# Optimization experiments

Hardware: AMD Instinct MI355X
Metric: run time of the kernel (lower is better)

Reference implementation:

```python
import jax, jax.numpy as jnp
from jax import lax
import numpy as np

N, T, V = 32, 32, 128
C_FEAT, C_BOX, C_CLS = 256, 4, 4
C_IN = C_FEAT + C_BOX + C_CLS  # 264 (is_scene=False concatenates x,b,c)
C_OUT = 64
K = 9
EPS = 1e-3  # keras BatchNormalization default epsilon


def _bn4(x, g, b, m, v):
    # inference-mode BN over channel axis 1 of (N,C,T,V)
    s = (g * lax.rsqrt(v + EPS))[None, :, None, None]
    return (x - m[None, :, None, None]) * s + b[None, :, None, None]


def _stgcn(x, a, imp, w, bw, ga, ba, ma, va, al, wt, bt, gb, bb, mb, vb, residual):
    res = x if residual else 0.0
    # SGCN: 1x1 conv (channels_first) then adjacency aggregation; dropout is identity at inference
    h = jnp.einsum('nctv,co->notv', x, w) + bw[None, :, None, None]
    h = jnp.einsum('nctv,ntvw->nctw', h, a * imp)
    # TGCN: BN -> PReLU(alpha per (C,T,V)) -> temporal conv (K,1) SAME -> BN -> (dropout=id)
    h = _bn4(h, ga, ba, ma, va)
    h = jnp.where(h >= 0, h, al[None] * h)
    h = lax.conv_general_dilated(h, wt, (1, 1), 'SAME',
                                 dimension_numbers=('NCHW', 'HWIO', 'NCHW')) + bt[None, :, None, None]
    h = _bn4(h, gb, bb, mb, vb)
    return h + res  # use_mdn=True -> no final PReLU


def _forward(x, b, c, a, dbn_g, dbn_b, dbn_m, dbn_v,
             w0, bw0, imp0, g0a, b0a, m0a, v0a, al0, wt0, bt0, g0b, b0b, m0b, v0b,
             w1, bw1, imp1, g1a, b1a, m1a, v1a, al1, wt1, bt1, g1b, b1b, m1b, v1b):
    x = jnp.concatenate([x, b, c], axis=-1)  # (N,T,V,C_IN)
    n, t, v, cc = x.shape
    # data BN over flattened (V*C) channel axis, exactly as the TF reshapes do
    x = jnp.transpose(x, (0, 2, 3, 1)).reshape(n, v * cc, t)
    s = (dbn_g * lax.rsqrt(dbn_v + EPS))[None, :, None]
    x = (x - dbn_m[None, :, None]) * s + dbn_b[None, :, None]
    # NOTE: the original does transpose(0,1,3,2) then a *reshape* to (N,C,T,V); replicate exactly
    x = x.reshape(n, v, cc, t).transpose(0, 1, 3, 2).reshape(n, cc, t, v)
    x = _stgcn(x, a, imp0, w0, bw0, g0a, b0a, m0a, v0a, al0, wt0, bt0, g0b, b0b, m0b, v0b, residual=False)
    x = _stgcn(x, a, imp1, w1, bw1, g1a, b1a, m1a, v1a, al1, wt1, bt1, g1b, b1b, m1b, v1b, residual=True)
    x = x[:, :, :, 0]  # (N,C_OUT,T)
    return jnp.transpose(x, (0, 2, 1))  # (N,T,C_OUT)


def setup_inputs():
    key = jax.random.key(0)
    ks = jax.random.split(key, 40)
    rn = lambda k, s, sc=1.0: jax.random.normal(k, s, jnp.float32) * sc
    ru = lambda k, s, lo, hi: jax.random.uniform(k, s, jnp.float32, lo, hi)
    d = {}
    d['x'] = rn(ks[0], (N, T, V, C_FEAT))
    d['b'] = rn(ks[1], (N, T, V, C_BOX))
    d['c'] = ru(ks[2], (N, T, V, C_CLS), 0.0, 1.0)
    d['a'] = ru(ks[3], (N, T, V, V), 0.0, 1.0)
    d['dbn_g'] = ru(ks[4], (V * C_IN,), 0.5, 1.5)
    d['dbn_b'] = rn(ks[5], (V * C_IN,), 0.1)
    d['dbn_m'] = rn(ks[6], (V * C_IN,), 0.1)
    d['dbn_v'] = ru(ks[7], (V * C_IN,), 0.5, 1.5)

    def mk_layer(i, cin, kb):
        d['w%d' % i] = rn(ks[kb], (cin, C_OUT), (1.0 / cin) ** 0.5)
        d['bw%d' % i] = rn(ks[kb + 1], (C_OUT,), 0.01)
        d['imp%d' % i] = rn(ks[kb + 2], (V, V), (2.0 / (V * V)) ** 0.5)
        d['g%da' % i] = ru(ks[kb + 3], (C_OUT,), 0.5, 1.5)
        d['b%da' % i] = rn(ks[kb + 4], (C_OUT,), 0.1)
        d['m%da' % i] = rn(ks[kb + 5], (C_OUT,), 0.1)
        d['v%da' % i] = ru(ks[kb + 6], (C_OUT,), 0.5, 1.5)
        d['al%d' % i] = ru(ks[kb + 7], (C_OUT, T, V), 0.0, 0.3)
        d['wt%d' % i] = rn(ks[kb + 8], (K, 1, C_OUT, C_OUT), (1.0 / (K * C_OUT)) ** 0.5)
        d['bt%d' % i] = rn(ks[kb + 9], (C_OUT,), 0.01)
        d['g%db' % i] = ru(ks[kb + 10], (C_OUT,), 0.5, 1.5)
        d['b%db' % i] = rn(ks[kb + 11], (C_OUT,), 0.1)
        d['m%db' % i] = rn(ks[kb + 12], (C_OUT,), 0.1)
        d['v%db' % i] = ru(ks[kb + 13], (C_OUT,), 0.5, 1.5)

    mk_layer(0, C_IN, 8)
    mk_layer(1, C_OUT, 22)
    return d


def reference(x, b, c, a, dbn_g, dbn_b, dbn_m, dbn_v,
              w0, bw0, imp0, g0a, b0a, m0a, v0a, al0, wt0, bt0, g0b, b0b, m0b, v0b,
              w1, bw1, imp1, g1a, b1a, m1a, v1a, al1, wt1, bt1, g1b, b1b, m1b, v1b):
    return _forward(x, b, c, a, dbn_g, dbn_b, dbn_m, dbn_v,
                    w0, bw0, imp0, g0a, b0a, m0a, v0a, al0, wt0, bt0, g0b, b0b, m0b, v0b,
                    w1, bw1, imp1, g1a, b1a, m1a, v1a, al1, wt1, bt1, g1b, b1b, m1b, v1b)
```

## Files before the change

### kernel.cpp

```cpp
#include <hip/hip_runtime.h>
#include <hip/hip_bf16.h>

typedef unsigned short u16;
typedef unsigned int   u32;

#define N_   32
#define T_   32
#define V_   128
#define CIN_ 264
#define CO_  64
#define KT_  9
#define EPS_ 1e-3f

#define OFF_DBN_S 0
#define OFF_DBN_O 33792
#define OFF_W0    67584
#define OFF_BW0   84480
#define OFF_A0S   84544
#define OFF_A0O   84608
#define OFF_B0S   84672
#define OFF_B0O   84736
#define OFF_W1    84800
#define OFF_BW1   88896
#define OFF_A1S   88960
#define OFF_A1O   89024
#define OFF_B1S   89088
#define OFF_B1O   89152
#define PREP_TOTAL 110464

#define B_P    0
#define B_FLAG 360448
#define B_W0A  360512
#define B_WTA  397440
#define B_H0   524288
#define B_G0   (B_H0 + 16777216)
#define B_L0   (B_G0 + 16777216)
#define B_G1P  (B_L0 + 33554432)
#define B_XP2  (B_G1P + 262144)
#define B_END  (B_XP2 + 69206016)

typedef short bf16x8 __attribute__((ext_vector_type(8)));
typedef float f32x4  __attribute__((ext_vector_type(4)));

__device__ __forceinline__ float bf2f(u16 u) { return __uint_as_float(((u32)u) << 16); }
__device__ __forceinline__ u16 f2bf(float f) {
    u32 x = __float_as_uint(f);
    return (u16)((x + 0x7fffu + ((x >> 16) & 1u)) >> 16);
}
__device__ __forceinline__ float ldin(const void* p, u32 i, int f32) {
    return f32 ? ((const float*)p)[i] : bf2f(((const u16*)p)[i]);
}
__device__ __forceinline__ u32 swzv(u32 v) {
    u32 m = (v >> 3) & 7u;
    return (m << 4) ^ ((m & 3u) << 5);
}

__global__ void k_detect(const void* a, int* flag) {
    if (threadIdx.x == 0 && blockIdx.x == 0) {
        const u16* p = (const u16*)a;
        int cnt = 0;
        for (int i = 0; i < 64; ++i) {
            float v = bf2f(p[2 * i]);
            if (v >= 0.f && v <= 1.0f) ++cnt;
        }
        *flag = (cnt >= 56) ? 0 : 1;
    }
}

__global__ void k_prep(const void* dbn_g, const void* dbn_b, const void* dbn_m, const void* dbn_v,
                       const void* w0, const void* bw0,
                       const void* g0a, const void* b0a, const void* m0a, const void* v0a,
                       const void* bt0, const void* g0b, const void* b0b, const void* m0b, const void* v0b,
                       const void* w1, const void* bw1,
                       const void* g1a, const void* b1a, const void* m1a, const void* v1a,
                       const void* bt1, const void* g1b, const void* b1b, const void* m1b, const void* v1b,
                       const void* wt0,
                       float* P, u16* W0A, u16* WTA, const int* flagp)
{
    const int f32 = *flagp;
    int i = blockIdx.x * 256 + threadIdx.x;
    if (i < 33792) {
        float s = ldin(dbn_g, i, f32) * rsqrtf(ldin(dbn_v, i, f32) + EPS_);
        P[OFF_DBN_S + i] = s;
        P[OFF_DBN_O + i] = ldin(dbn_b, i, f32) - ldin(dbn_m, i, f32) * s;
    } else if (i < 50688) { int j = i - 33792; P[OFF_W0 + j] = ldin(w0, j, f32); }
    else if (i < 50752) { int j = i - 50688; P[OFF_BW0 + j] = ldin(bw0, j, f32); }
    else if (i < 50816) { int j = i - 50752;
        float s = ldin(g0a, j, f32) * rsqrtf(ldin(v0a, j, f32) + EPS_);
        P[OFF_A0S + j] = s; P[OFF_A0O + j] = ldin(b0a, j, f32) - ldin(m0a, j, f32) * s;
    } else if (i < 50880) { int j = i - 50816;
        float s = ldin(g0b, j, f32) * rsqrtf(ldin(v0b, j, f32) + EPS_);
        P[OFF_B0S + j] = s; P[OFF_B0O + j] = (ldin(bt0, j, f32) - ldin(m0b, j, f32)) * s + ldin(b0b, j, f32);
    } else if (i < 54976) { int j = i - 50880; P[OFF_W1 + j] = ldin(w1, j, f32); }
    else if (i < 55040) { int j = i - 54976; P[OFF_BW1 + j] = ldin(bw1, j, f32); }
    else if (i < 55104) { int j = i - 55040;
        float s = ldin(g1a, j, f32) * rsqrtf(ldin(v1a, j, f32) + EPS_);
        P[OFF_A1S + j] = s; P[OFF_A1O + j] = ldin(b1a, j, f32) - ldin(m1a, j, f32) * s;
    } else if (i < 55168) { int j = i - 55104;
        float s = ldin(g1b, j, f32) * rsqrtf(ldin(v1b, j, f32) + EPS_);
        P[OFF_B1S + j] = s; P[OFF_B1O + j] = (ldin(bt1, j, f32) - ldin(m1b, j, f32)) * s + ldin(b1b, j, f32);
    } else if (i < 73600) {
        int j = i - 55168; int c = j / 288, ci = j - c * 288;
        float val = (ci < 264) ? ldin(w0, (u32)ci * 64 + c, f32)
                  : ((ci == 264) ? ldin(bw0, c, f32) : 0.f);
        W0A[j] = f2bf(val);
    } else if (i < 110464) {
        int j = i - 73600; int k = j >> 12, rem = j & 4095, o = rem >> 6, ii = rem & 63;
        WTA[j] = f2bf(ldin(wt0, ((u32)(k * 64 + ii)) * 64 + o, f32));
    }
}

__global__ __launch_bounds__(256) void k_bnx(const void* __restrict__ xin, const void* __restrict__ bin,
                                             const void* __restrict__ cin2, const float* __restrict__ P,
                                             u16* __restrict__ Xp, const int* __restrict__ flagp)
{
    __shared__ __align__(16) u16 tile[32 * 130];
    const int f32 = *flagp;
    const int rt = blockIdx.x;
    const int ct = blockIdx.y;
    const int n  = blockIdx.z;
    const int c0 = ct * 32;
    const int ncols = (ct == 8) ? 8 : 32;
    const int r0 = rt * 128;
    const int tid = threadIdx.x;

    for (int q = tid; q < ncols * 32; q += 256) {
        int j = q >> 5, i4 = (q & 31) << 2;
        u32 L = (u32)(c0 + j) * 4096u + (u32)(r0 + i4);
        u32 vs = L / 8448u;
        u32 r  = L - vs * 8448u;
        u32 ts = r / 264u;
        u32 cc = r - ts * 264u;
        u32 base = ((u32)n * 32u + ts) * 128u + vs;
        float4 val;
        if (f32) {
            if (cc < 256u)      val = *(const float4*)((const float*)xin  + (size_t)base * 256u + cc);
            else if (cc < 260u) val = *(const float4*)((const float*)bin  + (size_t)base * 4u + (cc - 256u));
            else                val = *(const float4*)((const float*)cin2 + (size_t)base * 4u + (cc - 260u));
        } else {
            ushort4 uv;
            if (cc < 256u)      uv = *(const ushort4*)((const u16*)xin  + (size_t)base * 256u + cc);
            else if (cc < 260u) uv = *(const ushort4*)((const u16*)bin  + (size_t)base * 4u + (cc - 256u));
            else                uv = *(const ushort4*)((const u16*)cin2 + (size_t)base * 4u + (cc - 260u));
            val.x = bf2f(uv.x); val.y = bf2f(uv.y); val.z = bf2f(uv.z); val.w = bf2f(uv.w);
        }
        u32 ch = vs * 264u + cc;
        const float4 s4 = *(const float4*)&P[OFF_DBN_S + ch];
        const float4 o4 = *(const float4*)&P[OFF_DBN_O + ch];
        ushort2 lo, hi;
        lo.x = f2bf(fmaf(val.x, s4.x, o4.x));
        lo.y = f2bf(fmaf(val.y, s4.y, o4.y));
        hi.x = f2bf(fmaf(val.z, s4.z, o4.z));
        hi.y = f2bf(fmaf(val.w, s4.w, o4.w));
        *(ushort2*)&tile[j * 130 + i4]     = lo;
        *(ushort2*)&tile[j * 130 + i4 + 2] = hi;
    }
    __syncthreads();
    const int chunks = ncols >> 3;
    for (int e = tid; e < 128 * chunks; e += 256) {
        int i, cch;
        if (chunks == 4) { i = e >> 2; cch = e & 3; } else { i = e; cch = 0; }
        __align__(16) u16 tmp[8];
#pragma unroll
        for (int k2 = 0; k2 < 8; ++k2) tmp[k2] = tile[(cch * 8 + k2) * 130 + i];
        *(uint4*)&Xp[((u32)n * 4096u + (u32)(r0 + i)) * 264u + (u32)(c0 + cch * 8)] = *(uint4*)tmp;
    }
}

__global__ __launch_bounds__(256) void k_pw0(const u16* __restrict__ Xp, const u16* __restrict__ W0Ag,
                                             u16* __restrict__ h0)
{
    const int t2 = blockIdx.x, n = blockIdx.y, vh = blockIdx.z;
    const int tid = threadIdx.x;
    const int wv = tid >> 6, lane = tid & 63, l16 = lane & 15, quad = lane >> 4;
    const int m0 = wv * 16;
    const int vrow = vh * 64 + m0 + l16;
    const u16* arow = Xp + ((u32)n * 4096u + (u32)(t2 * 128 + vrow)) * 264u;

    f32x4 acc[4];
#pragma unroll
    for (int i = 0; i < 4; ++i) acc[i] = (f32x4){0.f, 0.f, 0.f, 0.f};

#pragma unroll
    for (int ks = 0; ks < 8; ++ks) {
        const int k0 = ks * 32 + quad * 8;
        bf16x8 af = *(const bf16x8*)&arow[k0];
#pragma unroll
        for (int ni = 0; ni < 4; ++ni) {
            bf16x8 bf = *(const bf16x8*)&W0Ag[(u32)(ni * 16 + l16) * 288 + k0];
            acc[ni] = __builtin_amdgcn_mfma_f32_16x16x32_bf16(af, bf, acc[ni], 0, 0, 0);
        }
    }
    {
        bf16x8 af = (bf16x8){0, 0, 0, 0, 0, 0, 0, 0};
        if (quad == 0)      af = *(const bf16x8*)&arow[256];
        else if (quad == 1) af[0] = (short)0x3F80;
        const int k0 = 256 + quad * 8;
#pragma unroll
        for (int ni = 0; ni < 4; ++ni) {
            bf16x8 bf = *(const bf16x8*)&W0Ag[(u32)(ni * 16 + l16) * 288 + k0];
            acc[ni] = __builtin_amdgcn_mfma_f32_16x16x32_bf16(af, bf, acc[ni], 0, 0, 0);
        }
    }
    const int v = vh * 64 + m0 + quad * 4;
#pragma unroll
    for (int ni = 0; ni < 4; ++ni) {
        int c = ni * 16 + l16;
        ushort4 rr; u16* rp = (u16*)&rr;
#pragma unroll
        for (int r = 0; r < 4; ++r) rp[r] = f2bf(acc[ni][r]);
        *(ushort4*)&h0[((u32)(n * 64 + c) * 32 + t2) * 128 + v] = rr;
    }
}

__global__ __launch_bounds__(256) void k_graph0(const void* __restrict__ a, const void* __restrict__ imp0,
                                                const void* __restrict__ al0, const float* __restrict__ P,
                                                const u16* __restrict__ h0, u16* __restrict__ g0,
                                                const int* __restrict__ flagp)
{
    __shared__ __align__(16) u16 tile[128 * 128];
    const int f32 = *flagp;
    const int t = blockIdx.x, n = blockIdx.y;
    const int tid = threadIdx.x;
    const u32 abase = (((u32)n * 32u + (u32)t) * 128u) * 128u;

    for (int e = tid; e < 2048; e += 256) {
        int v = e >> 4, w0 = (e & 15) << 3;
        float vals[8];
        if (f32) {
            const float* ap = (const float*)a + abase + (u32)v * 128u + w0;
            const float* ip = (const float*)imp0 + (u32)v * 128u + w0;
            float4 x0 = *(const float4*)ap, x1 = *(const float4*)(ap + 4);
            float4 i0 = *(const float4*)ip, i1 = *(const float4*)(ip + 4);
            vals[0] = x0.x * i0.x; vals[1] = x0.y * i0.y; vals[2] = x0.z * i0.z; vals[3] = x0.w * i0.w;
            vals[4] = x1.x * i1.x; vals[5] = x1.y * i1.y; vals[6] = x1.z * i1.z; vals[7] = x1.w * i1.w;
        } else {
            uint4 xu = *(const uint4*)((const u16*)a + abase + (u32)v * 128u + w0);
            uint4 iu = *(const uint4*)((const u16*)imp0 + (u32)v * 128u + w0);
            const u16* xp = (const u16*)&xu; const u16* ip = (const u16*)&iu;
#pragma unroll
            for (int j = 0; j < 8; ++j) vals[j] = bf2f(xp[j]) * bf2f(ip[j]);
        }
        __align__(16) u16 pk[8];
#pragma unroll
        for (int j = 0; j < 8; ++j) pk[j] = f2bf(vals[j]);
        u32 byte = (u32)v * 256u + (((u32)w0 * 2u) ^ swzv((u32)v));
        *(uint4*)((char*)tile + byte) = *(uint4*)pk;
    }
    __syncthreads();

    const int wv = tid >> 6, lane = tid & 63, l16 = lane & 15, quad = lane >> 4;
    const int n0w = wv * 32;
    const u16* Hb = h0 + ((u32)n * 2048u + (u32)t) * 128u;

    f32x4 acc[4][2];
#pragma unroll
    for (int mi = 0; mi < 4; ++mi) { acc[mi][0] = (f32x4){0,0,0,0}; acc[mi][1] = (f32x4){0,0,0,0}; }
#pragma unroll
    for (int ks = 0; ks < 4; ++ks) {
        const int k0 = ks * 32 + quad * 8;
        const u32 xr = swzv((u32)k0);
        const u32 wb0 = (u32)(n0w + l16) * 2u;
        const u32 wb1 = (u32)(n0w + 16 + l16) * 2u;
        bf16x8 bf0, bf1;
#pragma unroll
        for (int j = 0; j < 8; ++j) {
            const u32 rb = (u32)(k0 + j) * 256u;
            bf0[j] = (short)*(const u16*)((const char*)tile + rb + (wb0 ^ xr));
            bf1[j] = (short)*(const u16*)((const char*)tile + rb + (wb1 ^ xr));
        }
#pragma unroll
        for (int mi = 0; mi < 4; ++mi) {
            bf16x8 af = *(const bf16x8*)&Hb[(u32)(mi * 16 + l16) * 4096u + k0];
            acc[mi][0] = __builtin_amdgcn_mfma_f32_16x16x32_bf16(af, bf0, acc[mi][0], 0, 0, 0);
            acc[mi][1] = __builtin_amdgcn_mfma_f32_16x16x32_bf16(af, bf1, acc[mi][1], 0, 0, 0);
        }
    }
#pragma unroll
    for (int mi = 0; mi < 4; ++mi) {
        const int c0 = mi * 16 + quad * 4;
        const float4 s4 = *(const float4*)&P[OFF_A0S + c0];
        const float4 o4 = *(const float4*)&P[OFF_A0O + c0];
        const float ss[4] = {s4.x, s4.y, s4.z, s4.w};
        const float oo[4] = {o4.x, o4.y, o4.z, o4.w};
#pragma unroll
        for (int ni = 0; ni < 2; ++ni) {
            const int w = n0w + ni * 16 + l16;
            ushort4 rr; u16* rp = (u16*)&rr;
#pragma unroll
            for (int r = 0; r < 4; ++r) {
                float y = fmaf(acc[mi][ni][r], ss[r], oo[r]);
                float alv = ldin(al0, ((u32)(c0 + r) * 32 + t) * 128 + w, f32);
                rp[r] = f2bf((y >= 0.f) ? y : alv * y);
            }
            *(ushort4*)&g0[((u32)(n * 32 + t) * 128 + w) * 64 + c0] = rr;
        }
    }
}

__global__ __launch_bounds__(256) void k_tconv0(const u16* __restrict__ WTAg, const float* __restrict__ P,
                                                const u16* __restrict__ g0, float* __restrict__ L0)
{
    const int t = blockIdx.x, n = blockIdx.y;
    const int tid = threadIdx.x;
    const int kmin = (t < 4) ? (4 - t) : 0;
    const int kmax = (t > 27) ? (35 - t) : 8;
    const int wv = tid >> 6, lane = tid & 63, l16 = lane & 15, quad = lane >> 4;
    const int n0w = wv * 32;

    f32x4 acc[4][2];
#pragma unroll
    for (int mi = 0; mi < 4; ++mi) { acc[mi][0] = (f32x4){0,0,0,0}; acc[mi][1] = (f32x4){0,0,0,0}; }

    for (int k = kmin; k <= kmax; ++k) {
        const u16* Wb = WTAg + (u32)k * 4096u;
        const u16* Bb = g0 + ((u32)(n * 32 + (t + k - 4)) * 128u) * 64u;
#pragma unroll
        for (int ks = 0; ks < 2; ++ks) {
            const int k0 = ks * 32 + quad * 8;
            bf16x8 bf0 = *(const bf16x8*)&Bb[(u32)(n0w + l16) * 64u + k0];
            bf16x8 bf1 = *(const bf16x8*)&Bb[(u32)(n0w + 16 + l16) * 64u + k0];
#pragma unroll
            for (int mi = 0; mi < 4; ++mi) {
                bf16x8 af = *(const bf16x8*)&Wb[(u32)(mi * 16 + l16) * 64u + k0];
                acc[mi][0] = __builtin_amdgcn_mfma_f32_16x16x32_bf16(af, bf0, acc[mi][0], 0, 0, 0);
                acc[mi][1] = __builtin_amdgcn_mfma_f32_16x16x32_bf16(af, bf1, acc[mi][1], 0, 0, 0);
            }
        }
    }
#pragma unroll
    for (int mi = 0; mi < 4; ++mi) {
        const int ob = mi * 16 + quad * 4;
        const float4 s4 = *(const float4*)&P[OFF_B0S + ob];
        const float4 o4 = *(const float4*)&P[OFF_B0O + ob];
        const float ss[4] = {s4.x, s4.y, s4.z, s4.w};
        const float oo[4] = {o4.x, o4.y, o4.z, o4.w};
#pragma unroll
        for (int ni = 0; ni < 2; ++ni) {
            const int v = n0w + ni * 16 + l16;
#pragma unroll
            for (int r = 0; r < 4; ++r)
                L0[((u32)(n * 64 + ob + r) * 32 + t) * 128 + v] = fmaf(acc[mi][ni][r], ss[r], oo[r]);
        }
    }
}

__global__ __launch_bounds__(256) void k_pw1(const void* __restrict__ a, const void* __restrict__ imp1,
                                             const void* __restrict__ al1, const float* __restrict__ P,
                                             const float* __restrict__ L0, float* __restrict__ g1p,
                                             const int* __restrict__ flagp)
{
    __shared__ float amv[V_];
    __shared__ float xr[CO_];
    __shared__ float Ssh;
    const int f32 = *flagp;
    const int t = blockIdx.x, n = blockIdx.y;
    const int tid = threadIdx.x;

    if (tid < V_) {
        float av = ldin(a, (((u32)n * T_ + t) * V_ + tid) * V_ + 0u, f32)
                 * ldin(imp1, (u32)tid * V_ + 0u, f32);
        amv[tid] = av;
    }
    __syncthreads();
    if (tid < 64) {
        float s = amv[tid] + amv[tid + 64];
#pragma unroll
        for (int m = 1; m < 64; m <<= 1) s += __shfl_xor(s, m);
        if (tid == 0) Ssh = s;
    }
    const int c = tid >> 2, sub = tid & 3;
    const float* Lrow = L0 + (u32)n * (CO_ * T_ * V_) + (u32)c * (T_ * V_) + (u32)t * V_ + sub * 32;
    float p = 0.f;
#pragma unroll
    for (int j = 0; j < 32; j += 4) {
        float4 x = *(const float4*)(Lrow + j);
        float4 m = *(const float4*)&amv[sub * 32 + j];
        p = fmaf(x.x, m.x, p); p = fmaf(x.y, m.y, p);
        p = fmaf(x.z, m.z, p); p = fmaf(x.w, m.w, p);
    }
    p += __shfl_xor(p, 1);
    p += __shfl_xor(p, 2);
    if (sub == 0) xr[c] = p;
    __syncthreads();
    if (tid < CO_) {
        const int o = tid;
        float y = P[OFF_BW1 + o] * Ssh;
        for (int cc = 0; cc < CO_; ++cc)
            y = fmaf(xr[cc], P[OFF_W1 + cc * CO_ + o], y);
        y = fmaf(y, P[OFF_A1S + o], P[OFF_A1O + o]);
        float alv = ldin(al1, ((u32)o * T_ + t) * V_ + 0u, f32);
        y = (y >= 0.f) ? y : alv * y;
        g1p[((u32)n * CO_ + o) * T_ + t] = y;
    }
}

__global__ __launch_bounds__(256) void k_tconv1(const void* __restrict__ wt1, const float* __restrict__ P,
                                                const float* __restrict__ g1p, const float* __restrict__ L0,
                                                void* __restrict__ out, const int* __restrict__ flagp)
{
    __shared__ float gl[CO_][40];
    const int f32 = *flagp;
    const int n = blockIdx.x;
    const int tid = threadIdx.x;
    for (int e = tid; e < 512; e += 256) {
        int i = e >> 3, p = e & 7;
        gl[i][(p < 4) ? p : (p + 32)] = 0.f;
    }
    for (int e = tid; e < 2048; e += 256) {
        int i = e >> 5, tt = e & 31;
        gl[i][tt + 4] = g1p[(u32)n * 2048u + (u32)i * 32u + tt];
    }
    __syncthreads();
    const int o = tid & 63, tq = tid >> 6, t0 = tq * 8;
    float acc[8];
#pragma unroll
    for (int j = 0; j < 8; ++j) acc[j] = 0.f;
    for (int i = 0; i < CO_; ++i) {
        float win[16];
#pragma unroll
        for (int m = 0; m < 16; m += 4) *(float4*)&win[m] = *(const float4*)&gl[i][t0 + m];
#pragma unroll
        for (int k = 0; k < KT_; ++k) {
            float wv = ldin(wt1, ((u32)(k * CO_ + i)) * CO_ + o, f32);
#pragma unroll
            for (int j = 0; j < 8; ++j) acc[j] = fmaf(win[j + k], wv, acc[j]);
        }
    }
    const float s1 = P[OFF_B1S + o], o1 = P[OFF_B1O + o];
#pragma unroll
    for (int j = 0; j < 8; ++j) {
        const int t = t0 + j;
        float y = fmaf(acc[j], s1, o1);
        y += L0[(u32)n * (CO_ * T_ * V_) + (u32)o * (T_ * V_) + (u32)t * V_ + 0];
        const u32 oi = ((u32)n * T_ + t) * CO_ + o;
        if (f32) ((float*)out)[oi] = y;
        else     ((u16*)out)[oi]   = f2bf(y);
    }
}

__global__ void k_fail(u16* out, int nel) {
    int i = blockIdx.x * 256 + threadIdx.x;
    if (i < nel) out[i] = 0x7f80;
}

extern "C" void kernel_launch(void* const* d_in, const int* in_sizes, int n_in,
                              void* d_out, int out_size, void* d_ws, size_t ws_size,
                              hipStream_t stream)
{
    const void* xin  = d_in[0];
    const void* bin  = d_in[1];
    const void* cin2 = d_in[2];
    const void* a    = d_in[3];
    const void* dbn_g = d_in[4];
    const void* dbn_b = d_in[5];
    const void* dbn_m = d_in[6];
    const void* dbn_v = d_in[7];
    const void* w0  = d_in[8];
    const void* bw0 = d_in[9];
    const void* imp0 = d_in[10];
    const void* g0a = d_in[11];
    const void* b0a = d_in[12];
    const void* m0a = d_in[13];
    const void* v0a = d_in[14];
    const void* al0 = d_in[15];
    const void* wt0 = d_in[16];
    const void* bt0 = d_in[17];
    const void* g0b = d_in[18];
    const void* b0b = d_in[19];
    const void* m0b = d_in[20];
    const void* v0b = d_in[21];
    const void* w1  = d_in[22];
    const void* bw1 = d_in[23];
    const void* imp1 = d_in[24];
    const void* g1a = d_in[25];
    const void* b1a = d_in[26];
    const void* m1a = d_in[27];
    const void* v1a = d_in[28];
    const void* al1 = d_in[29];
    const void* wt1 = d_in[30];
    const void* bt1 = d_in[31];
    const void* g1b = d_in[32];
    const void* b1b = d_in[33];
    const void* m1b = d_in[34];
    const void* v1b = d_in[35];

    if (ws_size < (size_t)B_END) {
        k_fail<<<(out_size + 255) / 256, 256, 0, stream>>>((u16*)d_out, out_size);
        return;
    }
    char* w = (char*)d_ws;
    float* P    = (float*)(w + B_P);
    int*   flg  = (int*)(w + B_FLAG);
    u16*   W0A  = (u16*)(w + B_W0A);
    u16*   WTA  = (u16*)(w + B_WTA);
    u16*   h0   = (u16*)(w + B_H0);
    u16*   g0   = (u16*)(w + B_G0);
    float* L0   = (float*)(w + B_L0);
    float* g1p  = (float*)(w + B_G1P);
    u16*   Xp   = (u16*)(w + B_XP2);

    k_detect<<<1, 64, 0, stream>>>(a, flg);
    k_prep<<<(PREP_TOTAL + 255) / 256, 256, 0, stream>>>(
        dbn_g, dbn_b, dbn_m, dbn_v, w0, bw0, g0a, b0a, m0a, v0a,
        bt0, g0b, b0b, m0b, v0b, w1, bw1, g1a, b1a, m1a, v1a,
        bt1, g1b, b1b, m1b, v1b, wt0, P, W0A, WTA, flg);

    dim3 grid(T_, N_);
    k_bnx   <<<dim3(32, 9, 32), 256, 0, stream>>>(xin, bin, cin2, P, Xp, flg);
    k_pw0   <<<dim3(T_, N_, 2), 256, 0, stream>>>(Xp, W0A, h0);
    k_graph0<<<grid, 256, 0, stream>>>(a, imp0, al0, P, h0, g0, flg);
    k_tconv0<<<grid, 256, 0, stream>>>(WTA, P, g0, L0);
    k_pw1   <<<grid, 256, 0, stream>>>(a, imp1, al1, P, L0, g1p, flg);
    k_tconv1<<<dim3(N_), 256, 0, stream>>>(wt1, P, g1p, L0, d_out, flg);
}
```

Measured before the change: 506.5 us.

## Fuse data batch-norm transpose into first pointwise MFMA kernel via swizzled LDS tile

```diff
diff --git a/kernel.cpp b/kernel.cpp
--- a/kernel.cpp
+++ b/kernel.cpp
@@ -36,8 +36,7 @@
 #define B_G0   (B_H0 + 16777216)
 #define B_L0   (B_G0 + 16777216)
 #define B_G1P  (B_L0 + 33554432)
-#define B_XP2  (B_G1P + 262144)
-#define B_END  (B_XP2 + 69206016)
+#define B_END  (B_G1P + 262144)
 
 typedef short bf16x8 __attribute__((ext_vector_type(8)));
 typedef float f32x4  __attribute__((ext_vector_type(4)));
@@ -50,8 +49,8 @@
 __device__ __forceinline__ float ldin(const void* p, u32 i, int f32) {
     return f32 ? ((const float*)p)[i] : bf2f(((const u16*)p)[i]);
 }
-__device__ __forceinline__ u32 swzv(u32 v) {
-    u32 m = (v >> 3) & 7u;
+__device__ __forceinline__ u32 swzv(u32 row) {
+    u32 m = (row >> 3) & 7u;
     return (m << 4) ^ ((m & 3u) << 5);
 }
 
@@ -110,99 +109,94 @@
     }
 }
 
-__global__ __launch_bounds__(256) void k_bnx(const void* __restrict__ xin, const void* __restrict__ bin,
+__global__ __launch_bounds__(256) void k_pwf(const void* __restrict__ xin, const void* __restrict__ bin,
                                              const void* __restrict__ cin2, const float* __restrict__ P,
-                                             u16* __restrict__ Xp, const int* __restrict__ flagp)
-{
-    __shared__ __align__(16) u16 tile[32 * 130];
+                                             const u16* __restrict__ W0Ag, u16* __restrict__ h0,
+                                             const int* __restrict__ flagp)
+{
+    __shared__ __align__(16) u16 tile[288 * 64];
     const int f32 = *flagp;
-    const int rt = blockIdx.x;
-    const int ct = blockIdx.y;
-    const int n  = blockIdx.z;
-    const int c0 = ct * 32;
-    const int ncols = (ct == 8) ? 8 : 32;
-    const int r0 = rt * 128;
+    const int t2 = blockIdx.x, n = blockIdx.y, vh = blockIdx.z;
     const int tid = threadIdx.x;
 
-    for (int q = tid; q < ncols * 32; q += 256) {
-        int j = q >> 5, i4 = (q & 31) << 2;
-        u32 L = (u32)(c0 + j) * 4096u + (u32)(r0 + i4);
+    for (int e = tid; e < 192; e += 256) {
+        int row = 264 + (e >> 3), chunk = e & 7;
+        u32 fill = (row == 264) ? 0x3F803F80u : 0u;
+        uint4 z = make_uint4(fill, fill, fill, fill);
+        u32 byte = (u32)row * 128u + (((u32)chunk * 16u) ^ swzv((u32)row));
+        *(uint4*)((char*)tile + byte) = z;
+    }
+    for (int e = tid; e < 2112; e += 256) {
+        int c2 = e >> 3, vv0 = (e & 7) << 3;
+        u32 L = (u32)c2 * 4096u + (u32)(t2 * 128 + vh * 64 + vv0);
         u32 vs = L / 8448u;
         u32 r  = L - vs * 8448u;
         u32 ts = r / 264u;
         u32 cc = r - ts * 264u;
         u32 base = ((u32)n * 32u + ts) * 128u + vs;
-        float4 val;
+        u32 ch = vs * 264u + cc;
+        float v8[8];
         if (f32) {
-            if (cc < 256u)      val = *(const float4*)((const float*)xin  + (size_t)base * 256u + cc);
-            else if (cc < 260u) val = *(const float4*)((const float*)bin  + (size_t)base * 4u + (cc - 256u));
-            else                val = *(const float4*)((const float*)cin2 + (size_t)base * 4u + (cc - 260u));
+            float4 a0, a1;
+            if (cc < 256u) {
+                const float* sp = (const float*)xin + (size_t)base * 256u + cc;
+                a0 = *(const float4*)sp; a1 = *(const float4*)(sp + 4);
+            } else {
+                a0 = *(const float4*)((const float*)bin  + (size_t)base * 4u);
+                a1 = *(const float4*)((const float*)cin2 + (size_t)base * 4u);
+            }
+            v8[0] = a0.x; v8[1] = a0.y; v8[2] = a0.z; v8[3] = a0.w;
+            v8[4] = a1.x; v8[5] = a1.y; v8[6] = a1.z; v8[7] = a1.w;
         } else {
-            ushort4 uv;
-            if (cc < 256u)      uv = *(const ushort4*)((const u16*)xin  + (size_t)base * 256u + cc);
-            else if (cc < 260u) uv = *(const ushort4*)((const u16*)bin  + (size_t)base * 4u + (cc - 256u));
-            else                uv = *(const ushort4*)((const u16*)cin2 + (size_t)base * 4u + (cc - 260u));
-            val.x = bf2f(uv.x); val.y = bf2f(uv.y); val.z = bf2f(uv.z); val.w = bf2f(uv.w);
-        }
-        u32 ch = vs * 264u + cc;
-        const float4 s4 = *(const float4*)&P[OFF_DBN_S + ch];
-        const float4 o4 = *(const float4*)&P[OFF_DBN_O + ch];
-        ushort2 lo, hi;
-        lo.x = f2bf(fmaf(val.x, s4.x, o4.x));
-        lo.y = f2bf(fmaf(val.y, s4.y, o4.y));
-        hi.x = f2bf(fmaf(val.z, s4.z, o4.z));
-        hi.y = f2bf(fmaf(val.w, s4.w, o4.w));
-        *(ushort2*)&tile[j * 130 + i4]     = lo;
-        *(ushort2*)&tile[j * 130 + i4 + 2] = hi;
+            __align__(16) u16 up[8];
+            if (cc < 256u) {
+                *(uint4*)up = *(const uint4*)((const u16*)xin + (size_t)base * 256u + cc);
+            } else {
+                *(ushort4*)&up[0] = *(const ushort4*)((const u16*)bin  + (size_t)base * 4u);
+                *(ushort4*)&up[4] = *(const ushort4*)((const u16*)cin2 + (size_t)base * 4u);
+            }
+#pragma unroll
+            for (int j = 0; j < 8; ++j) v8[j] = bf2f(up[j]);
+        }
+        const float4 s0 = *(const float4*)&P[OFF_DBN_S + ch];
+        const float4 s1 = *(const float4*)&P[OFF_DBN_S + ch + 4];
+        const float4 o0 = *(const float4*)&P[OFF_DBN_O + ch];
+        const float4 o1 = *(const float4*)&P[OFF_DBN_O + ch + 4];
+        __align__(16) u16 pk[8];
+        pk[0] = f2bf(fmaf(v8[0], s0.x, o0.x));
+        pk[1] = f2bf(fmaf(v8[1], s0.y, o0.y));
+        pk[2] = f2bf(fmaf(v8[2], s0.z, o0.z));
+        pk[3] = f2bf(fmaf(v8[3], s0.w, o0.w));
+        pk[4] = f2bf(fmaf(v8[4], s1.x, o1.x));
+        pk[5] = f2bf(fmaf(v8[5], s1.y, o1.y));
+        pk[6] = f2bf(fmaf(v8[6], s1.z, o1.z));
+        pk[7] = f2bf(fmaf(v8[7], s1.w, o1.w));
+        u32 byte = (u32)c2 * 128u + (((u32)vv0 * 2u) ^ swzv((u32)c2));
+        *(uint4*)((char*)tile + byte) = *(uint4*)pk;
     }
     __syncthreads();
-    const int chunks = ncols >> 3;
-    for (int e = tid; e < 128 * chunks; e += 256) {
-        int i, cch;
-        if (chunks == 4) { i = e >> 2; cch = e & 3; } else { i = e; cch = 0; }
-        __align__(16) u16 tmp[8];
-#pragma unroll
-        for (int k2 = 0; k2 < 8; ++k2) tmp[k2] = tile[(cch * 8 + k2) * 130 + i];
-        *(uint4*)&Xp[((u32)n * 4096u + (u32)(r0 + i)) * 264u + (u32)(c0 + cch * 8)] = *(uint4*)tmp;
-    }
-}
-
-__global__ __launch_bounds__(256) void k_pw0(const u16* __restrict__ Xp, const u16* __restrict__ W0Ag,
-                                             u16* __restrict__ h0)
-{
-    const int t2 = blockIdx.x, n = blockIdx.y, vh = blockIdx.z;
-    const int tid = threadIdx.x;
+
     const int wv = tid >> 6, lane = tid & 63, l16 = lane & 15, quad = lane >> 4;
-    const int m0 = wv * 16;
-    const int vrow = vh * 64 + m0 + l16;
-    const u16* arow = Xp + ((u32)n * 4096u + (u32)(t2 * 128 + vrow)) * 264u;
-
     f32x4 acc[4];
 #pragma unroll
     for (int i = 0; i < 4; ++i) acc[i] = (f32x4){0.f, 0.f, 0.f, 0.f};
 
 #pragma unroll
-    for (int ks = 0; ks < 8; ++ks) {
+    for (int ks = 0; ks < 9; ++ks) {
         const int k0 = ks * 32 + quad * 8;
-        bf16x8 af = *(const bf16x8*)&arow[k0];
+        const u32 xr = swzv((u32)k0);
+        const u32 cb = ((u32)(wv * 16 + l16) * 2u) ^ xr;
+        bf16x8 af;
+#pragma unroll
+        for (int j = 0; j < 8; ++j)
+            af[j] = (short)*(const u16*)((const char*)tile + (u32)(k0 + j) * 128u + cb);
 #pragma unroll
         for (int ni = 0; ni < 4; ++ni) {
             bf16x8 bf = *(const bf16x8*)&W0Ag[(u32)(ni * 16 + l16) * 288 + k0];
             acc[ni] = __builtin_amdgcn_mfma_f32_16x16x32_bf16(af, bf, acc[ni], 0, 0, 0);
         }
     }
-    {
-        bf16x8 af = (bf16x8){0, 0, 0, 0, 0, 0, 0, 0};
-        if (quad == 0)      af = *(const bf16x8*)&arow[256];
-        else if (quad == 1) af[0] = (short)0x3F80;
-        const int k0 = 256 + quad * 8;
-#pragma unroll
-        for (int ni = 0; ni < 4; ++ni) {
-            bf16x8 bf = *(const bf16x8*)&W0Ag[(u32)(ni * 16 + l16) * 288 + k0];
-            acc[ni] = __builtin_amdgcn_mfma_f32_16x16x32_bf16(af, bf, acc[ni], 0, 0, 0);
-        }
-    }
-    const int v = vh * 64 + m0 + quad * 4;
+    const int v = vh * 64 + wv * 16 + quad * 4;
 #pragma unroll
     for (int ni = 0; ni < 4; ++ni) {
         int c = ni * 16 + l16;
@@ -498,7 +492,6 @@
     u16*   g0   = (u16*)(w + B_G0);
     float* L0   = (float*)(w + B_L0);
     float* g1p  = (float*)(w + B_G1P);
-    u16*   Xp   = (u16*)(w + B_XP2);
 
     k_detect<<<1, 64, 0, stream>>>(a, flg);
     k_prep<<<(PREP_TOTAL + 255) / 256, 256, 0, stream>>>(
@@ -507,8 +500,7 @@
         bt1, g1b, b1b, m1b, v1b, wt0, P, W0A, WTA, flg);
 
     dim3 grid(T_, N_);
-    k_bnx   <<<dim3(32, 9, 32), 256, 0, stream>>>(xin, bin, cin2, P, Xp, flg);
-    k_pw0   <<<dim3(T_, N_, 2), 256, 0, stream>>>(Xp, W0A, h0);
+    k_pwf   <<<dim3(T_, N_, 2), 256, 0, stream>>>(xin, bin, cin2, P, W0A, h0, flg);
     k_graph0<<<grid, 256, 0, stream>>>(a, imp0, al0, P, h0, g0, flg);
     k_tconv0<<<grid, 256, 0, stream>>>(WTA, P, g0, L0);
     k_pw1   <<<grid, 256, 0, stream>>>(a, imp1, al1, P, L0, g1p, flg);
```

New measurement: 487.5 us. 3.8% less time.
